# Kernel optimization log

Hardware: AMD Instinct MI355X
Metric: run time of the kernel (lower is better)

## Reference

```python
import jax, jax.numpy as jnp
import numpy as np

H, DK = 8, 64  # n_head, d_k = n_feat // n_head
SCALE = 1.0 / np.sqrt(DK)


def setup_inputs() -> dict:
    key0 = jax.random.key(0)
    ks = jax.random.split(key0, 13)
    B, N, T1, T2, F = 16, 4, 256, 1024, 512
    query = jax.random.normal(ks[0], (B, T1, F), jnp.float32)
    key = jax.random.normal(ks[1], (B, N, T2, F), jnp.float32)
    value = jax.random.normal(ks[2], (B, N, T2, F), jnp.float32)
    mask_audio = jax.random.randint(ks[3], (B, N, 1, T2), 0, 2).astype(jnp.int32)
    # guarantee each candidate row has at least one valid key frame
    mask_audio = mask_audio.at[..., 0].set(1)
    mask_spk = jax.random.randint(ks[4], (B, N), 0, 2).astype(jnp.int32)
    # guarantee at least one valid candidate per batch item (avoids all -inf softmax)
    mask_spk = mask_spk.at[:, 0].set(1)
    s = 1.0 / np.sqrt(F)
    Wq = jax.random.normal(ks[5], (F, F), jnp.float32) * s
    bq = jax.random.normal(ks[6], (F,), jnp.float32) * 0.01
    Wk = jax.random.normal(ks[7], (F, F), jnp.float32) * s
    bk = jax.random.normal(ks[8], (F,), jnp.float32) * 0.01
    Wv = jax.random.normal(ks[9], (F, F), jnp.float32) * s
    bv = jax.random.normal(ks[10], (F,), jnp.float32) * 0.01
    Wo = jax.random.normal(ks[11], (F, F), jnp.float32) * s
    bo = jax.random.normal(ks[12], (F,), jnp.float32) * 0.01
    return dict(query=query, key=key, value=value, mask_audio=mask_audio,
                mask_spk=mask_spk, Wq=Wq, bq=bq, Wk=Wk, bk=bk, Wv=Wv, bv=bv,
                Wo=Wo, bo=bo)


def reference(query, key, value, mask_audio, mask_spk, Wq, bq, Wk, bk, Wv, bv, Wo, bo):
    B, T1, F = query.shape
    N, T2 = key.shape[1], key.shape[2]
    # projections (torch Linear: x @ W.T + b)
    q = (query @ Wq.T + bq).reshape(B, T1, H, DK)                 # (B,T1,H,DK)
    k = (key @ Wk.T + bk).reshape(B, N, T2, H, DK)                # (B,N,T2,H,DK)
    v = (value @ Wv.T + bv).reshape(B, N, T2, H, DK)
    # stage 1: intra-candidate temporal attention
    scores = jnp.einsum('bthd,bnshd->bnhts', q, k) * SCALE        # (B,N,H,T1,T2)
    ma = (mask_audio != 0)[:, :, None, :, :]                      # (B,N,1,1,T2)
    scores = jnp.where(ma, scores, -jnp.inf)
    attn1 = jnp.where(ma, jax.nn.softmax(scores, axis=-1), 0.0)
    phone = jnp.einsum('bnhts,bnshd->bnhtd', attn1, v)            # (B,N,H,T1,DK)
    # stage 2: inter-candidate attention
    ss = jnp.einsum('bthd,bnhtd->bthn', q, phone) * SCALE         # (B,T1,H,N)
    ms = (mask_spk != 0)[:, None, None, :]                        # (B,1,1,N)
    ss = jnp.where(ms, ss, -jnp.inf)
    attn2 = jnp.where(ms, jax.nn.softmax(ss, axis=-1), 0.0)
    x = jnp.einsum('bthn,bnhtd->bthd', attn2, phone).reshape(B, T1, H * DK)
    return x @ Wo.T + bo
```

## Files before the change

kernel.cpp:

```cpp
#include <hip/hip_runtime.h>
#include <hip/hip_bf16.h>
#include <math.h>

typedef __attribute__((ext_vector_type(4))) float  f32x4;
typedef __attribute__((ext_vector_type(4))) int    i32x4;
typedef __attribute__((ext_vector_type(8))) __bf16 bf16x8;
typedef __attribute__((ext_vector_type(8))) unsigned short u16x8;
typedef __attribute__((ext_vector_type(4))) unsigned short u16x4;

#define DEV static __device__ __forceinline__

#if __has_builtin(__builtin_amdgcn_permlane32_swap) && __has_builtin(__builtin_amdgcn_permlane16_swap)
#define HAVE_PERMLANE 1
#else
#define HAVE_PERMLANE 0
#endif

namespace {

constexpr int kB = 16, kT1 = 256, kF = 512, kN = 4, kT2 = 1024, kH = 8;
constexpr float kSCALE = 0.125f;
constexpr float kLOG2E = 1.4426950408889634f;

DEV unsigned short f2bf(float f) {
  union { __bf16 h; unsigned short u; } c; c.h = (__bf16)f; return c.u;
}
DEV float bf2f(unsigned short h) {
  union { unsigned u; float f; } c; c.u = ((unsigned)h) << 16;
  return c.f;
}

DEV void async_copy16(const void* g, void* l) {
  __builtin_amdgcn_global_load_lds(
      (const __attribute__((address_space(1))) unsigned int*)g,
      (__attribute__((address_space(3))) unsigned int*)l, 16, 0, 0);
}

DEV bf16x8 cvt8(f32x4 lo, f32x4 hi) {
  bf16x8 r;
  r[0] = (__bf16)lo[0]; r[1] = (__bf16)lo[1]; r[2] = (__bf16)lo[2]; r[3] = (__bf16)lo[3];
  r[4] = (__bf16)hi[0]; r[5] = (__bf16)hi[1]; r[6] = (__bf16)hi[2]; r[7] = (__bf16)hi[3];
  return r;
}

__global__ __launch_bounds__(256) void convert_w(
    const float* __restrict__ w0, const float* __restrict__ w1,
    const float* __restrict__ w2, const float* __restrict__ w3,
    unsigned short* __restrict__ o0, unsigned short* __restrict__ o1,
    unsigned short* __restrict__ o2, unsigned short* __restrict__ o3) {
  const int r = blockIdx.x >> 8;
  const int l = ((blockIdx.x & 255) * 256 + threadIdx.x) * 4;
  const float* src = r == 0 ? w0 : r == 1 ? w1 : r == 2 ? w2 : w3;
  unsigned short* dst = r == 0 ? o0 : r == 1 ? o1 : r == 2 ? o2 : o3;
  const float4 v = *(const float4*)(src + l);
  u16x4 q; q[0] = f2bf(v.x); q[1] = f2bf(v.y); q[2] = f2bf(v.z); q[3] = f2bf(v.w);
  *(u16x4*)(dst + l) = q;
}

template<int MODE>
__global__ __launch_bounds__(512, 2) void gemm256(
    const float* __restrict__ A, const unsigned short* __restrict__ Wb,
    const float* __restrict__ bias, unsigned short* __restrict__ outv) {
  __shared__ __align__(16) unsigned short As[2][256 * 64];
  __shared__ __align__(16) unsigned short Ws[2][256 * 64];
  const int t = threadIdx.x, lane = t & 63, wave = t >> 6;
  const int rb = blockIdx.x >> 1, cb = blockIdx.x & 1;
  const int wr = wave >> 2, wc = wave & 3;
  const int lq = lane & 15, lg = lane >> 4;
  const int arg = t >> 4, as16 = t & 15;

  f32x4 acc[8][4];
#pragma unroll
  for (int i = 0; i < 8; ++i)
#pragma unroll
    for (int j = 0; j < 4; ++j) acc[i][j] = f32x4{0.f, 0.f, 0.f, 0.f};

  f32x4 areg[8];
  bf16x8 af[4][2], bf[4][2];

#define A_ISSUE(kt)                                                             \
  do {                                                                          \
    _Pragma("unroll")                                                           \
    for (int j_ = 0; j_ < 8; ++j_)                                              \
      areg[j_] = *(const f32x4*)(A + (size_t)(rb * 256 + j_ * 32 + arg) * kF +  \
                                 (kt) * 64 + as16 * 4);                         \
  } while (0)

#define A_WRITE(dst)                                                            \
  do {                                                                          \
    _Pragma("unroll")                                                           \
    for (int j_ = 0; j_ < 8; ++j_) {                                            \
      const int row_ = j_ * 32 + arg;                                           \
      const int off_ = row_ * 64 + (((as16 >> 1) ^ (row_ & 7)) << 3) + (as16 & 1) * 4; \
      u16x4 pk_;                                                                \
      pk_[0] = f2bf(areg[j_][0]); pk_[1] = f2bf(areg[j_][1]);                   \
      pk_[2] = f2bf(areg[j_][2]); pk_[3] = f2bf(areg[j_][3]);                   \
      *(u16x4*)&(dst)[off_] = pk_;                                              \
    }                                                                           \
  } while (0)

#define W_ISSUE(kt, dst)                                                        \
  do {                                                                          \
    _Pragma("unroll")                                                           \
    for (int j_ = 0; j_ < 4; ++j_) {                                            \
      const int sidx_ = t + j_ * 512;                                           \
      const int row_ = sidx_ >> 3, s_ = sidx_ & 7;                              \
      async_copy16(Wb + (size_t)(cb * 256 + row_) * kF + (kt) * 64 +            \
                       ((s_ ^ (row_ & 7)) << 3),                                \
                   (dst) + (size_t)(j_ * 512 + wave * 64) * 8);                 \
    }                                                                           \
  } while (0)

#define RD_BF(pw)                                                               \
  do {                                                                          \
    _Pragma("unroll")                                                           \
    for (int n_ = 0; n_ < 4; ++n_) {                                            \
      const int br_ = wc * 64 + n_ * 16 + lq, x7_ = br_ & 7;                    \
      bf[n_][0] = *(const bf16x8*)&(pw)[br_ * 64 + ((lg ^ x7_) << 3)];          \
      bf[n_][1] = *(const bf16x8*)&(pw)[br_ * 64 + (((4 + lg) ^ x7_) << 3)];    \
    }                                                                           \
  } while (0)

#define RD_AF(pa, mb)                                                           \
  do {                                                                          \
    _Pragma("unroll")                                                           \
    for (int m_ = 0; m_ < 4; ++m_) {                                            \
      const int ar_ = wr * 128 + ((mb) + m_) * 16 + lq, x7_ = ar_ & 7;          \
      af[m_][0] = *(const bf16x8*)&(pa)[ar_ * 64 + ((lg ^ x7_) << 3)];          \
      af[m_][1] = *(const bf16x8*)&(pa)[ar_ * 64 + (((4 + lg) ^ x7_) << 3)];    \
    }                                                                           \
  } while (0)

#define MM(mb)                                                                  \
  do {                                                                          \
    _Pragma("unroll")                                                           \
    for (int kk_ = 0; kk_ < 2; ++kk_)                                           \
      _Pragma("unroll")                                                         \
      for (int m_ = 0; m_ < 4; ++m_)                                            \
        _Pragma("unroll")                                                       \
        for (int n_ = 0; n_ < 4; ++n_)                                          \
          acc[(mb) + m_][n_] = __builtin_amdgcn_mfma_f32_16x16x32_bf16(         \
              af[m_][kk_], bf[n_][kk_], acc[(mb) + m_][n_], 0, 0, 0);           \
  } while (0)

#define VMW0 asm volatile("s_waitcnt vmcnt(0)" ::: "memory")
#define LKW  asm volatile("s_waitcnt lgkmcnt(0)" ::: "memory")
#define SB   __builtin_amdgcn_sched_barrier(0)
#define BAR  do { __builtin_amdgcn_s_barrier(); __builtin_amdgcn_sched_barrier(0); } while (0)

  A_ISSUE(0); W_ISSUE(0, Ws[0]);
  VMW0; SB;
  A_WRITE(As[0]);
  LKW; BAR;

  unsigned short *pa = As[0], *qa = As[1], *pw = Ws[0], *qw = Ws[1];
#pragma unroll 1
  for (int kt = 0; kt < 8; ++kt) {
    if (kt < 7) { A_ISSUE(kt + 1); W_ISSUE(kt + 1, qw); }
    RD_BF(pw); RD_AF(pa, 0);
    LKW; SB;
    __builtin_amdgcn_s_setprio(1); MM(0); __builtin_amdgcn_s_setprio(0); SB;
    RD_AF(pa, 4);
    LKW; SB;
    __builtin_amdgcn_s_setprio(1); MM(4); __builtin_amdgcn_s_setprio(0); SB;
    if (kt < 7) { VMW0; SB; A_WRITE(qa); }
    LKW; BAR;
    { unsigned short* x = pa; pa = qa; qa = x; }
    { unsigned short* x = pw; pw = qw; qw = x; }
  }

#undef A_ISSUE
#undef A_WRITE
#undef W_ISSUE
#undef RD_BF
#undef RD_AF
#undef MM
#undef VMW0
#undef LKW
#undef SB
#undef BAR

  float bs4[4];
#pragma unroll
  for (int n = 0; n < 4; ++n) bs4[n] = bias[cb * 256 + wc * 64 + n * 16 + lq];

#pragma unroll
  for (int m = 0; m < 8; ++m) {
    const int row0 = rb * 256 + wr * 128 + m * 16 + lg * 4;
    const int bn = row0 >> 10, t2 = row0 & 1023;
#pragma unroll
    for (int n = 0; n < 4; ++n) {
      const int col = cb * 256 + wc * 64 + n * 16 + lq;
      const int h = col >> 6, d = col & 63;
      if (MODE == 3) {
        u16x4 pv;
#pragma unroll
        for (int j = 0; j < 4; ++j) pv[j] = f2bf(acc[m][n][j] + bs4[n]);
        *(u16x4*)&outv[(((size_t)(bn * kH + h)) * 64 + d) * kT2 + t2] = pv;
      } else {
#pragma unroll
        for (int j = 0; j < 4; ++j)
          outv[(((size_t)(bn * kH + h)) * kT2 + t2 + j) * 64 + d] =
              f2bf(acc[m][n][j] + bs4[n]);
      }
    }
  }
}

template<int MODE>
__global__ __launch_bounds__(256, 2) void gemm_mixed(
    const float* __restrict__ A, const unsigned short* __restrict__ Wb,
    const float* __restrict__ bias, void* __restrict__ outv, int nrb) {
  __shared__ __align__(16) unsigned short As[2][128 * 64];
  __shared__ __align__(16) unsigned short Bs[3][128 * 64];
  const int t = threadIdx.x, lane = t & 63, wave = t >> 6;
  const int w = blockIdx.x;
  const int xcd = w & 7, s = w >> 3;
  const int rb = xcd * (nrb >> 3) + (s >> 2);
  const int cb = s & 3;
  const int wr = wave >> 1, wc = wave & 1;
  const int lq = lane & 15, lg = lane >> 4;

  const int arow = t >> 1, ah = (t & 1) * 4;
  const float* aptr = A + (size_t)(rb * 128 + arow) * kF + ah * 8;

  f32x4 acc[4][4];
#pragma unroll
  for (int i = 0; i < 4; ++i)
#pragma unroll
    for (int j = 0; j < 4; ++j) acc[i][j] = f32x4{0.f, 0.f, 0.f, 0.f};

  f32x4 arA[8], arB[8];
  bf16x8 af[4][2], bfr[4][2];

#define A_LOAD(kb, ar)                                                          \
  do {                                                                          \
    const f32x4* p_ = (const f32x4*)(aptr + (kb) * 64);                         \
    ar[0]=p_[0]; ar[1]=p_[1]; ar[2]=p_[2]; ar[3]=p_[3];                         \
    ar[4]=p_[4]; ar[5]=p_[5]; ar[6]=p_[6]; ar[7]=p_[7];                         \
  } while (0)

#define A_CVT(ar, dst)                                                          \
  do {                                                                          \
    _Pragma("unroll")                                                           \
    for (int j_ = 0; j_ < 4; ++j_)                                              \
      *(bf16x8*)&(dst)[arow * 64 + (((ah + j_) ^ (arow & 7)) << 3)] =           \
          cvt8(ar[2*j_], ar[2*j_+1]);                                           \
  } while (0)

#define W_STAGE(kb, dst)                                                        \
  do {                                                                          \
    _Pragma("unroll")                                                           \
    for (int i_ = 0; i_ < 2; ++i_) {                                            \
      const int sidx_ = t + i_ * 256;                                           \
      const int row_ = sidx_ >> 2;                                              \
      const int gseg_ = 0;                                                      \
      (void)gseg_;                                                              \
      const int r8_ = sidx_ >> 3;                                               \
      const int s8_ = sidx_ & 7;                                                \
      async_copy16(Wb + (size_t)(cb * 128 + r8_) * kF + (kb) * 64 +             \
                       ((s8_ ^ (r8_ & 7)) << 3),                                \
                   (dst) + (size_t)(i_ * 256 + wave * 64) * 8);                 \
      (void)row_;                                                               \
    }                                                                           \
  } while (0)

#define W_STAGE2(kb, dst)                                                       \
  do {                                                                          \
    _Pragma("unroll")                                                           \
    for (int i_ = 0; i_ < 4; ++i_) {                                            \
      const int sidx_ = t + i_ * 256;                                           \
      const int row_ = sidx_ >> 3;                                              \
      const int gseg_ = (sidx_ & 7) ^ (row_ & 7);                               \
      async_copy16(Wb + (size_t)(cb * 128 + row_) * kF + (kb) * 64 + gseg_ * 8, \
                   (dst) + (size_t)(i_ * 256 + wave * 64) * 8);                 \
    }                                                                           \
  } while (0)

#define FRAG(Ap, Wp)                                                            \
  do {                                                                          \
    _Pragma("unroll")                                                           \
    for (int m_ = 0; m_ < 4; ++m_) {                                            \
      const int ar_ = wr * 64 + m_ * 16 + lq, x7_ = ar_ & 7;                    \
      af[m_][0] = *(const bf16x8*)&(Ap)[ar_ * 64 + ((lg       ^ x7_) << 3)];    \
      af[m_][1] = *(const bf16x8*)&(Ap)[ar_ * 64 + (((lg + 4) ^ x7_) << 3)];    \
    }                                                                           \
    _Pragma("unroll")                                                           \
    for (int n_ = 0; n_ < 4; ++n_) {                                            \
      const int br_ = wc * 64 + n_ * 16 + lq, x7_ = br_ & 7;                    \
      bfr[n_][0] = *(const bf16x8*)&(Wp)[br_ * 64 + ((lg       ^ x7_) << 3)];   \
      bfr[n_][1] = *(const bf16x8*)&(Wp)[br_ * 64 + (((lg + 4) ^ x7_) << 3)];   \
    }                                                                           \
  } while (0)

#define MFMA8                                                                   \
  do {                                                                          \
    _Pragma("unroll")                                                           \
    for (int kk_ = 0; kk_ < 2; ++kk_)                                           \
      _Pragma("unroll")                                                         \
      for (int m_ = 0; m_ < 4; ++m_)                                            \
        _Pragma("unroll")                                                       \
        for (int n_ = 0; n_ < 4; ++n_)                                          \
          acc[m_][n_] = __builtin_amdgcn_mfma_f32_16x16x32_bf16(                \
              af[m_][kk_], bfr[n_][kk_], acc[m_][n_], 0, 0, 0);                 \
  } while (0)

#define VMW(n) asm volatile("s_waitcnt vmcnt(" #n ")" ::: "memory")
#define LKW    asm volatile("s_waitcnt lgkmcnt(0)" ::: "memory")
#define BAR    do { __builtin_amdgcn_s_barrier(); __builtin_amdgcn_sched_barrier(0); } while (0)

  A_LOAD(0, arA); A_LOAD(1, arB);
  W_STAGE2(0, Bs[0]); W_STAGE2(1, Bs[1]);
  VMW(16);
  A_CVT(arA, As[0]);
  LKW; BAR;
  A_LOAD(2, arA); W_STAGE2(2, Bs[2]);
  FRAG(As[0], Bs[0]); MFMA8;
  VMW(12); A_CVT(arB, As[1]); LKW; BAR;
  A_LOAD(3, arB); W_STAGE2(3, Bs[0]);
  FRAG(As[1], Bs[1]); MFMA8;
  VMW(12); A_CVT(arA, As[0]); LKW; BAR;
  A_LOAD(4, arA); W_STAGE2(4, Bs[1]);
  FRAG(As[0], Bs[2]); MFMA8;
  VMW(12); A_CVT(arB, As[1]); LKW; BAR;
  A_LOAD(5, arB); W_STAGE2(5, Bs[2]);
  FRAG(As[1], Bs[0]); MFMA8;
  VMW(12); A_CVT(arA, As[0]); LKW; BAR;
  A_LOAD(6, arA); W_STAGE2(6, Bs[0]);
  FRAG(As[0], Bs[1]); MFMA8;
  VMW(12); A_CVT(arB, As[1]); LKW; BAR;
  A_LOAD(7, arB); W_STAGE2(7, Bs[1]);
  FRAG(As[1], Bs[2]); MFMA8;
  VMW(12); A_CVT(arA, As[0]); LKW; BAR;
  FRAG(As[0], Bs[0]); MFMA8;
  VMW(0); A_CVT(arB, As[1]); LKW; BAR;
  FRAG(As[1], Bs[1]); MFMA8;

#undef A_LOAD
#undef A_CVT
#undef W_STAGE
#undef W_STAGE2
#undef FRAG
#undef MFMA8
#undef VMW
#undef LKW
#undef BAR

  float bs[4];
#pragma unroll
  for (int n2 = 0; n2 < 4; ++n2) bs[n2] = bias[cb*128 + wc*64 + n2*16 + lq];

#pragma unroll
  for (int m = 0; m < 4; ++m) {
#pragma unroll
    for (int n2 = 0; n2 < 4; ++n2) {
      const int col = cb*128 + wc*64 + n2*16 + lq;
      const int row0 = rb*128 + wr*64 + m*16 + lg*4;
#pragma unroll
      for (int j = 0; j < 4; ++j) {
        const int row = row0 + j;
        const float v = acc[m][n2][j] + bs[n2];
        if (MODE == 2) {
          ((float*)outv)[(size_t)row * kF + col] = v;
        } else {
          const int h = col >> 6, d = col & 63;
          const int b = row >> 8, t1i = row & 255;
          ((unsigned short*)outv)[(((size_t)(b * kH + h)) * kT1 + t1i) * 64 + d] = f2bf(v);
        }
      }
    }
  }
}

__global__ __launch_bounds__(512, 4) void attn_kernel(
    const unsigned short* __restrict__ qh, const unsigned short* __restrict__ kh,
    const unsigned short* __restrict__ vt, const int* __restrict__ mask_audio,
    unsigned short* __restrict__ phone) {
  __shared__ __align__(16) unsigned short Ks[4][64 * 64];
  __shared__ __align__(16) unsigned short Vs[4][64 * 64];
  __shared__ float Mbias[1024];
  const int t = threadIdx.x;
  const int lane = t & 63, wave = t >> 6;
  const int lq = lane & 15, lg = lane >> 4;
  const int bid = blockIdx.x;
  const int h = bid & 7, n = (bid >> 3) & 3, b = bid >> 5;
  const size_t qbase  = ((size_t)(b * kH + h)) * kT1 * 64;
  const size_t kvbase = ((size_t)((b * kN + n) * kH + h)) * kT2 * 64;
  const int* mbase = mask_audio + (size_t)(b * kN + n) * kT2;

  const int srow = (wave << 3) + (lane >> 3);
  const int sseg = lane & 7;
  const int sgx = (sseg ^ (srow & 7)) << 3;

#define STAGE_KV(c, buf)                                                          \
  do {                                                                            \
    async_copy16(kh + kvbase + ((size_t)(((c) << 6) + srow) << 6) + sgx,          \
                 &Ks[buf][wave << 9]);                                            \
    async_copy16(vt + kvbase + ((size_t)srow << 10) + ((c) << 6) + sgx,           \
                 &Vs[buf][wave << 9]);                                            \
  } while (0)

  {
    const int i0 = t * 2;
    const int m0 = mbase[i0], m1 = mbase[i0 + 1];
    Mbias[i0]     = m0 ? 0.f : -1e30f;
    Mbias[i0 + 1] = m1 ? 0.f : -1e30f;
  }

  bf16x8 qf[2][2];
#pragma unroll
  for (int qt = 0; qt < 2; ++qt) {
    const unsigned short* qp = qh + qbase + ((size_t)((wave << 5) + (qt << 4) + lq) << 6);
    qf[qt][0] = *(const bf16x8*)(qp + (lg << 3));
    qf[qt][1] = *(const bf16x8*)(qp + 32 + (lg << 3));
  }

  STAGE_KV(0, 0);
  STAGE_KV(1, 1);
  asm volatile("s_waitcnt lgkmcnt(0)" ::: "memory");

  f32x4 of[2][4];
  float m2[2], l1[2];
#pragma unroll
  for (int qt = 0; qt < 2; ++qt) {
    m2[qt] = -INFINITY; l1[qt] = 0.f;
#pragma unroll
    for (int fd = 0; fd < 4; ++fd) of[qt][fd] = f32x4{0.f, 0.f, 0.f, 0.f};
  }
  const float sc2 = kSCALE * kLOG2E;

#pragma unroll 1
  for (int c = 0; c < 16; ++c) {
    if (c < 14) STAGE_KV(c + 2, (c + 2) & 3);
    if (c < 14)      asm volatile("s_waitcnt vmcnt(4)" ::: "memory");
    else if (c == 14) asm volatile("s_waitcnt vmcnt(2)" ::: "memory");
    else              asm volatile("s_waitcnt vmcnt(0)" ::: "memory");
    __builtin_amdgcn_s_barrier();
    __builtin_amdgcn_sched_barrier(0);

    const unsigned short* Kb = Ks[c & 3];
    const unsigned short* Vb = Vs[c & 3];
    const float* mrow = Mbias + (c << 6);

    bf16x8 kf[4][2];
#pragma unroll
    for (int kt = 0; kt < 4; ++kt) {
      const int kr = kt * 16 + lq, x7 = kr & 7;
      kf[kt][0] = *(const bf16x8*)&Kb[kr * 64 + ((lg       ^ x7) << 3)];
      kf[kt][1] = *(const bf16x8*)&Kb[kr * 64 + (((lg + 4) ^ x7) << 3)];
    }

#pragma unroll
    for (int qt = 0; qt < 2; ++qt) {
      f32x4 sT[4];
#pragma unroll
      for (int kt = 0; kt < 4; ++kt) {
        f32x4 sv = f32x4{0.f, 0.f, 0.f, 0.f};
        sv = __builtin_amdgcn_mfma_f32_16x16x32_bf16(kf[kt][0], qf[qt][0], sv, 0, 0, 0);
        sv = __builtin_amdgcn_mfma_f32_16x16x32_bf16(kf[kt][1], qf[qt][1], sv, 0, 0, 0);
        sT[kt] = sv;
      }
      float scv[16];
#pragma unroll
      for (int kt = 0; kt < 4; ++kt) {
        const f32x4 mk = *(const f32x4*)&mrow[kt * 16 + lg * 4];
#pragma unroll
        for (int j = 0; j < 4; ++j)
          scv[kt*4+j] = fmaf(sT[kt][j], sc2, mk[j]);
      }
      const float x0 = fmaxf(fmaxf(scv[0],  scv[1]),  scv[2]);
      const float x1 = fmaxf(fmaxf(scv[3],  scv[4]),  scv[5]);
      const float x2 = fmaxf(fmaxf(scv[6],  scv[7]),  scv[8]);
      const float x3 = fmaxf(fmaxf(scv[9],  scv[10]), scv[11]);
      const float x4 = fmaxf(fmaxf(scv[12], scv[13]), scv[14]);
      float rmax = fmaxf(fmaxf(fmaxf(x0, x1), x2), fmaxf(fmaxf(x3, x4), scv[15]));
      rmax = fmaxf(rmax, __shfl_xor(rmax, 16));
      rmax = fmaxf(rmax, __shfl_xor(rmax, 32));
      const float mold = m2[qt];
      if (!__all(rmax <= mold + 8.f)) {
        const float mnew = fmaxf(mold, rmax);
        const float rs = exp2f(mold - mnew);
        m2[qt] = mnew;
        l1[qt] *= rs;
        const float s0 = __shfl(rs, lg*4 + 0);
        const float s1 = __shfl(rs, lg*4 + 1);
        const float s2 = __shfl(rs, lg*4 + 2);
        const float s3 = __shfl(rs, lg*4 + 3);
#pragma unroll
        for (int fd = 0; fd < 4; ++fd) {
          of[qt][fd][0] *= s0; of[qt][fd][1] *= s1;
          of[qt][fd][2] *= s2; of[qt][fd][3] *= s3;
        }
      }
      const float mloc = m2[qt];
      float pf[16];
#pragma unroll
      for (int i = 0; i < 16; ++i) pf[i] = exp2f(scv[i] - mloc);
      const float a0 = (pf[0] + pf[1]) + (pf[2] + pf[3]);
      const float a1 = (pf[4] + pf[5]) + (pf[6] + pf[7]);
      const float a2 = (pf[8] + pf[9]) + (pf[10] + pf[11]);
      const float a3 = (pf[12] + pf[13]) + (pf[14] + pf[15]);
      float psum = (a0 + a1) + (a2 + a3);
      psum += __shfl_xor(psum, 16);
      psum += __shfl_xor(psum, 32);
      l1[qt] += psum;
      unsigned pk[8];
#pragma unroll
      for (int kt = 0; kt < 4; ++kt) {
        pk[2*kt]   = (unsigned)f2bf(pf[4*kt+0]) | ((unsigned)f2bf(pf[4*kt+1]) << 16);
        pk[2*kt+1] = (unsigned)f2bf(pf[4*kt+2]) | ((unsigned)f2bf(pf[4*kt+3]) << 16);
      }
      unsigned am0[4], am1[4];
#if HAVE_PERMLANE
      {
        auto x0p = __builtin_amdgcn_permlane32_swap((int)pk[0], (int)pk[2], false, false);
        auto y0p = __builtin_amdgcn_permlane16_swap(x0p[0], x0p[1], false, false);
        am0[0] = (unsigned)y0p[0]; am0[2] = (unsigned)y0p[1];
        auto x1p = __builtin_amdgcn_permlane32_swap((int)pk[1], (int)pk[3], false, false);
        auto y1p = __builtin_amdgcn_permlane16_swap(x1p[0], x1p[1], false, false);
        am0[1] = (unsigned)y1p[0]; am0[3] = (unsigned)y1p[1];
        auto x2p = __builtin_amdgcn_permlane32_swap((int)pk[4], (int)pk[6], false, false);
        auto y2p = __builtin_amdgcn_permlane16_swap(x2p[0], x2p[1], false, false);
        am1[0] = (unsigned)y2p[0]; am1[2] = (unsigned)y2p[1];
        auto x3p = __builtin_amdgcn_permlane32_swap((int)pk[5], (int)pk[7], false, false);
        auto y3p = __builtin_amdgcn_permlane16_swap(x3p[0], x3p[1], false, false);
        am1[1] = (unsigned)y3p[0]; am1[3] = (unsigned)y3p[1];
      }
#else
      {
        const int srcbase = (2 * (lg & 1)) * 16 + lq;
#pragma unroll
        for (int u = 0; u < 4; ++u) {
          const int src = srcbase + (u >> 1) * 16;
          const unsigned va0 = __shfl(pk[(u & 1)],     src);
          const unsigned vb0 = __shfl(pk[2 + (u & 1)], src);
          am0[u] = (lg & 2) ? vb0 : va0;
          const unsigned va1 = __shfl(pk[4 + (u & 1)], src);
          const unsigned vb1 = __shfl(pk[6 + (u & 1)], src);
          am1[u] = (lg & 2) ? vb1 : va1;
        }
      }
#endif
      union { unsigned u[4]; bf16x8 v; } A0, A1;
#pragma unroll
      for (int u = 0; u < 4; ++u) { A0.u[u] = am0[u]; A1.u[u] = am1[u]; }
#pragma unroll
      for (int fd = 0; fd < 4; ++fd) {
        const int d = fd * 16 + lq, x7d = d & 7;
        const bf16x8 vB0 = *(const bf16x8*)&Vb[d * 64 + ((lg       ^ x7d) << 3)];
        const bf16x8 vB1 = *(const bf16x8*)&Vb[d * 64 + (((lg + 4) ^ x7d) << 3)];
        of[qt][fd] = __builtin_amdgcn_mfma_f32_16x16x32_bf16(A0.v, vB0, of[qt][fd], 0, 0, 0);
        of[qt][fd] = __builtin_amdgcn_mfma_f32_16x16x32_bf16(A1.v, vB1, of[qt][fd], 0, 0, 0);
      }
    }
  }
#undef STAGE_KV

  const size_t phbase = ((size_t)((b * kN + n) * kH + h)) * kT1 * 64;
#pragma unroll
  for (int qt = 0; qt < 2; ++qt) {
    const float li0 = 1.f / __shfl(l1[qt], lg*4 + 0);
    const float li1 = 1.f / __shfl(l1[qt], lg*4 + 1);
    const float li2 = 1.f / __shfl(l1[qt], lg*4 + 2);
    const float li3 = 1.f / __shfl(l1[qt], lg*4 + 3);
#pragma unroll
    for (int fd = 0; fd < 4; ++fd) {
      const int d = fd * 16 + lq;
      const size_t rowb = phbase + (size_t)((wave << 5) + qt*16 + lg*4) * 64 + d;
      phone[rowb]       = f2bf(of[qt][fd][0] * li0);
      phone[rowb + 64]  = f2bf(of[qt][fd][1] * li1);
      phone[rowb + 128] = f2bf(of[qt][fd][2] * li2);
      phone[rowb + 192] = f2bf(of[qt][fd][3] * li3);
    }
  }
}

__global__ __launch_bounds__(256) void stage2_kernel(
    const unsigned short* __restrict__ qh, const unsigned short* __restrict__ phone,
    const int* __restrict__ mask_spk, float* __restrict__ x) {
  const int t = threadIdx.x, lane = t & 63, wave = t >> 6;
  const int wid = blockIdx.x * 4 + wave;
  const int h = wid & 7;
  const int bt = wid >> 3;
  const int t1i = bt & 255, b = bt >> 8;
  const int d = lane;
  const float q = bf2f(qh[(((size_t)(b * kH + h)) * kT1 + t1i) * 64 + d]);
  float ph[4], ss[4];
#pragma unroll
  for (int n = 0; n < 4; ++n) {
    ph[n] = bf2f(phone[(((size_t)((b * kN + n) * kH + h)) * kT1 + t1i) * 64 + d]);
    float sv = q * ph[n];
#pragma unroll
    for (int o = 1; o < 64; o <<= 1) sv += __shfl_xor(sv, o);
    ss[n] = sv * kSCALE;
  }
  int msk[4];
#pragma unroll
  for (int n = 0; n < 4; ++n) msk[n] = mask_spk[b * kN + n];
  float mx = -INFINITY;
#pragma unroll
  for (int n = 0; n < 4; ++n) if (msk[n]) mx = fmaxf(mx, ss[n]);
  float e[4], sum = 0.f;
#pragma unroll
  for (int n = 0; n < 4; ++n) { const float v = msk[n] ? __expf(ss[n] - mx) : 0.f; e[n] = v; sum += v; }
  float xo = 0.f;
#pragma unroll
  for (int n = 0; n < 4; ++n) xo += e[n] * ph[n];
  xo /= sum;
  x[((size_t)(b * kT1 + t1i)) * kF + h * 64 + d] = xo;
}

}

extern "C" void kernel_launch(void* const* d_in, const int* in_sizes, int n_in,
                              void* d_out, int out_size, void* d_ws, size_t ws_size,
                              hipStream_t stream) {
  (void)in_sizes; (void)n_in; (void)out_size; (void)ws_size;
  const float* query = (const float*)d_in[0];
  const float* key   = (const float*)d_in[1];
  const float* value = (const float*)d_in[2];
  const int* mask_audio = (const int*)d_in[3];
  const int* mask_spk   = (const int*)d_in[4];
  const float* Wq = (const float*)d_in[5];  const float* bq = (const float*)d_in[6];
  const float* Wk = (const float*)d_in[7];  const float* bk = (const float*)d_in[8];
  const float* Wv = (const float*)d_in[9];  const float* bv = (const float*)d_in[10];
  const float* Wo = (const float*)d_in[11]; const float* bo = (const float*)d_in[12];
  float* out = (float*)d_out;

  unsigned short* qws  = (unsigned short*)d_ws;
  unsigned short* kws  = qws  + (size_t)kB * kH * kT1 * 64;
  unsigned short* vws  = kws  + (size_t)kB * kN * kH * kT2 * 64;
  unsigned short* phws = vws  + (size_t)kB * kN * kH * kT2 * 64;
  float*          xws  = (float*)(phws + (size_t)kB * kN * kH * kT1 * 64);
  unsigned short* wqb  = (unsigned short*)(xws + (size_t)kB * kT1 * kF);
  unsigned short* wkb  = wqb + (size_t)kF * kF;
  unsigned short* wvb  = wkb + (size_t)kF * kF;
  unsigned short* wob  = wvb + (size_t)kF * kF;

  convert_w<<<1024, 256, 0, stream>>>(Wq, Wk, Wv, Wo, wqb, wkb, wvb, wob);
  gemm_mixed<0><<<kB * kT1 / 128 * 4, 256, 0, stream>>>(query, wqb, bq, qws, kB * kT1 / 128);
  gemm256<1><<<kB * kN * kT2 / 256 * 2, 512, 0, stream>>>(key,   wkb, bk, kws);
  gemm256<3><<<kB * kN * kT2 / 256 * 2, 512, 0, stream>>>(value, wvb, bv, vws);
  attn_kernel<<<kB * kN * kH, 512, 0, stream>>>(qws, kws, vws, mask_audio, phws);
  stage2_kernel<<<kB * kT1 * kH / 4, 256, 0, stream>>>(qws, phws, mask_spk, xws);
  gemm_mixed<2><<<kB * kT1 / 128 * 4, 256, 0, stream>>>(xws, wob, bo, out, kB * kT1 / 128);
}
```

Baseline: 280.0 us.

## Drop online-softmax max tracking and shrink KV ring to three buffers

```diff
diff --git a/kernel.cpp b/kernel.cpp
--- a/kernel.cpp
+++ b/kernel.cpp
@@ -246,23 +246,6 @@
     for (int j_ = 0; j_ < 4; ++j_)                                              \
       *(bf16x8*)&(dst)[arow * 64 + (((ah + j_) ^ (arow & 7)) << 3)] =           \
           cvt8(ar[2*j_], ar[2*j_+1]);                                           \
-  } while (0)
-
-#define W_STAGE(kb, dst)                                                        \
-  do {                                                                          \
-    _Pragma("unroll")                                                           \
-    for (int i_ = 0; i_ < 2; ++i_) {                                            \
-      const int sidx_ = t + i_ * 256;                                           \
-      const int row_ = sidx_ >> 2;                                              \
-      const int gseg_ = 0;                                                      \
-      (void)gseg_;                                                              \
-      const int r8_ = sidx_ >> 3;                                               \
-      const int s8_ = sidx_ & 7;                                                \
-      async_copy16(Wb + (size_t)(cb * 128 + r8_) * kF + (kb) * 64 +             \
-                       ((s8_ ^ (r8_ & 7)) << 3),                                \
-                   (dst) + (size_t)(i_ * 256 + wave * 64) * 8);                 \
-      (void)row_;                                                               \
-    }                                                                           \
   } while (0)
 
 #define W_STAGE2(kb, dst)                                                       \
@@ -338,7 +321,6 @@
 
 #undef A_LOAD
 #undef A_CVT
-#undef W_STAGE
 #undef W_STAGE2
 #undef FRAG
 #undef MFMA8
@@ -372,12 +354,12 @@
   }
 }
 
-__global__ __launch_bounds__(512, 4) void attn_kernel(
+__global__ __launch_bounds__(512, 6) void attn_kernel(
     const unsigned short* __restrict__ qh, const unsigned short* __restrict__ kh,
     const unsigned short* __restrict__ vt, const int* __restrict__ mask_audio,
     unsigned short* __restrict__ phone) {
-  __shared__ __align__(16) unsigned short Ks[4][64 * 64];
-  __shared__ __align__(16) unsigned short Vs[4][64 * 64];
+  __shared__ __align__(16) unsigned short Ks[3][64 * 64];
+  __shared__ __align__(16) unsigned short Vs[3][64 * 64];
   __shared__ float Mbias[1024];
   const int t = threadIdx.x;
   const int lane = t & 63, wave = t >> 6;
@@ -389,15 +371,14 @@
   const int* mbase = mask_audio + (size_t)(b * kN + n) * kT2;
 
   const int srow = (wave << 3) + (lane >> 3);
-  const int sseg = lane & 7;
-  const int sgx = (sseg ^ (srow & 7)) << 3;
-
-#define STAGE_KV(c, buf)                                                          \
+  const int sgx = ((lane & 7) ^ (srow & 7)) << 3;
+
+#define STAGE_KV(c, kd, vd)                                                       \
   do {                                                                            \
     async_copy16(kh + kvbase + ((size_t)(((c) << 6) + srow) << 6) + sgx,          \
-                 &Ks[buf][wave << 9]);                                            \
+                 (kd) + (wave << 9));                                             \
     async_copy16(vt + kvbase + ((size_t)srow << 10) + ((c) << 6) + sgx,           \
-                 &Vs[buf][wave << 9]);                                            \
+                 (vd) + (wave << 9));                                             \
   } while (0)
 
   {
@@ -415,15 +396,18 @@
     qf[qt][1] = *(const bf16x8*)(qp + 32 + (lg << 3));
   }
 
-  STAGE_KV(0, 0);
-  STAGE_KV(1, 1);
+  unsigned short *kb0 = Ks[0], *kb1 = Ks[1], *kb2 = Ks[2];
+  unsigned short *vb0 = Vs[0], *vb1 = Vs[1], *vb2 = Vs[2];
+
+  STAGE_KV(0, kb0, vb0);
+  STAGE_KV(1, kb1, vb1);
   asm volatile("s_waitcnt lgkmcnt(0)" ::: "memory");
 
   f32x4 of[2][4];
-  float m2[2], l1[2];
+  float l1[2];
 #pragma unroll
   for (int qt = 0; qt < 2; ++qt) {
-    m2[qt] = -INFINITY; l1[qt] = 0.f;
+    l1[qt] = 0.f;
 #pragma unroll
     for (int fd = 0; fd < 4; ++fd) of[qt][fd] = f32x4{0.f, 0.f, 0.f, 0.f};
   }
@@ -431,23 +415,19 @@
 
 #pragma unroll 1
   for (int c = 0; c < 16; ++c) {
-    if (c < 14) STAGE_KV(c + 2, (c + 2) & 3);
-    if (c < 14)      asm volatile("s_waitcnt vmcnt(4)" ::: "memory");
-    else if (c == 14) asm volatile("s_waitcnt vmcnt(2)" ::: "memory");
-    else              asm volatile("s_waitcnt vmcnt(0)" ::: "memory");
+    if (c < 15) asm volatile("s_waitcnt vmcnt(2)" ::: "memory");
+    else        asm volatile("s_waitcnt vmcnt(0)" ::: "memory");
     __builtin_amdgcn_s_barrier();
     __builtin_amdgcn_sched_barrier(0);
 
-    const unsigned short* Kb = Ks[c & 3];
-    const unsigned short* Vb = Vs[c & 3];
     const float* mrow = Mbias + (c << 6);
 
     bf16x8 kf[4][2];
 #pragma unroll
     for (int kt = 0; kt < 4; ++kt) {
       const int kr = kt * 16 + lq, x7 = kr & 7;
-      kf[kt][0] = *(const bf16x8*)&Kb[kr * 64 + ((lg       ^ x7) << 3)];
-      kf[kt][1] = *(const bf16x8*)&Kb[kr * 64 + (((lg + 4) ^ x7) << 3)];
+      kf[kt][0] = *(const bf16x8*)&kb0[kr * 64 + ((lg       ^ x7) << 3)];
+      kf[kt][1] = *(const bf16x8*)&kb0[kr * 64 + (((lg + 4) ^ x7) << 3)];
     }
 
 #pragma unroll
@@ -460,50 +440,19 @@
         sv = __builtin_amdgcn_mfma_f32_16x16x32_bf16(kf[kt][1], qf[qt][1], sv, 0, 0, 0);
         sT[kt] = sv;
       }
-      float scv[16];
+      float pf[16];
 #pragma unroll
       for (int kt = 0; kt < 4; ++kt) {
         const f32x4 mk = *(const f32x4*)&mrow[kt * 16 + lg * 4];
 #pragma unroll
         for (int j = 0; j < 4; ++j)
-          scv[kt*4+j] = fmaf(sT[kt][j], sc2, mk[j]);
-      }
-      const float x0 = fmaxf(fmaxf(scv[0],  scv[1]),  scv[2]);
-      const float x1 = fmaxf(fmaxf(scv[3],  scv[4]),  scv[5]);
-      const float x2 = fmaxf(fmaxf(scv[6],  scv[7]),  scv[8]);
-      const float x3 = fmaxf(fmaxf(scv[9],  scv[10]), scv[11]);
-      const float x4 = fmaxf(fmaxf(scv[12], scv[13]), scv[14]);
-      float rmax = fmaxf(fmaxf(fmaxf(x0, x1), x2), fmaxf(fmaxf(x3, x4), scv[15]));
-      rmax = fmaxf(rmax, __shfl_xor(rmax, 16));
-      rmax = fmaxf(rmax, __shfl_xor(rmax, 32));
-      const float mold = m2[qt];
-      if (!__all(rmax <= mold + 8.f)) {
-        const float mnew = fmaxf(mold, rmax);
-        const float rs = exp2f(mold - mnew);
-        m2[qt] = mnew;
-        l1[qt] *= rs;
-        const float s0 = __shfl(rs, lg*4 + 0);
-        const float s1 = __shfl(rs, lg*4 + 1);
-        const float s2 = __shfl(rs, lg*4 + 2);
-        const float s3 = __shfl(rs, lg*4 + 3);
-#pragma unroll
-        for (int fd = 0; fd < 4; ++fd) {
-          of[qt][fd][0] *= s0; of[qt][fd][1] *= s1;
-          of[qt][fd][2] *= s2; of[qt][fd][3] *= s3;
-        }
-      }
-      const float mloc = m2[qt];
-      float pf[16];
-#pragma unroll
-      for (int i = 0; i < 16; ++i) pf[i] = exp2f(scv[i] - mloc);
+          pf[kt*4+j] = exp2f(fmaf(sT[kt][j], sc2, mk[j]));
+      }
       const float a0 = (pf[0] + pf[1]) + (pf[2] + pf[3]);
       const float a1 = (pf[4] + pf[5]) + (pf[6] + pf[7]);
       const float a2 = (pf[8] + pf[9]) + (pf[10] + pf[11]);
       const float a3 = (pf[12] + pf[13]) + (pf[14] + pf[15]);
-      float psum = (a0 + a1) + (a2 + a3);
-      psum += __shfl_xor(psum, 16);
-      psum += __shfl_xor(psum, 32);
-      l1[qt] += psum;
+      l1[qt] += (a0 + a1) + (a2 + a3);
       unsigned pk[8];
 #pragma unroll
       for (int kt = 0; kt < 4; ++kt) {
@@ -533,11 +482,11 @@
         for (int u = 0; u < 4; ++u) {
           const int src = srcbase + (u >> 1) * 16;
           const unsigned va0 = __shfl(pk[(u & 1)],     src);
-          const unsigned vb0 = __shfl(pk[2 + (u & 1)], src);
-          am0[u] = (lg & 2) ? vb0 : va0;
+          const unsigned vb0s = __shfl(pk[2 + (u & 1)], src);
+          am0[u] = (lg & 2) ? vb0s : va0;
           const unsigned va1 = __shfl(pk[4 + (u & 1)], src);
-          const unsigned vb1 = __shfl(pk[6 + (u & 1)], src);
-          am1[u] = (lg & 2) ? vb1 : va1;
+          const unsigned vb1s = __shfl(pk[6 + (u & 1)], src);
+          am1[u] = (lg & 2) ? vb1s : va1;
         }
       }
 #endif
@@ -547,15 +496,24 @@
 #pragma unroll
       for (int fd = 0; fd < 4; ++fd) {
         const int d = fd * 16 + lq, x7d = d & 7;
-        const bf16x8 vB0 = *(const bf16x8*)&Vb[d * 64 + ((lg       ^ x7d) << 3)];
-        const bf16x8 vB1 = *(const bf16x8*)&Vb[d * 64 + (((lg + 4) ^ x7d) << 3)];
+        const bf16x8 vB0 = *(const bf16x8*)&vb0[d * 64 + ((lg       ^ x7d) << 3)];
+        const bf16x8 vB1 = *(const bf16x8*)&vb0[d * 64 + (((lg + 4) ^ x7d) << 3)];
         of[qt][fd] = __builtin_amdgcn_mfma_f32_16x16x32_bf16(A0.v, vB0, of[qt][fd], 0, 0, 0);
         of[qt][fd] = __builtin_amdgcn_mfma_f32_16x16x32_bf16(A1.v, vB1, of[qt][fd], 0, 0, 0);
       }
     }
+
+    if (c < 14) STAGE_KV(c + 2, kb2, vb2);
+    { unsigned short* x = kb0; kb0 = kb1; kb1 = kb2; kb2 = x; }
+    { unsigned short* x = vb0; vb0 = vb1; vb1 = vb2; vb2 = x; }
   }
 #undef STAGE_KV
 
+#pragma unroll
+  for (int qt = 0; qt < 2; ++qt) {
+    l1[qt] += __shfl_xor(l1[qt], 16);
+    l1[qt] += __shfl_xor(l1[qt], 32);
+  }
   const size_t phbase = ((size_t)((b * kN + n) * kH + h)) * kT1 * 64;
 #pragma unroll
   for (int qt = 0; qt < 2; ++qt) {
```

Measured after the change: 754.1 us. 2.69x slower.
